# Performance work log

Hardware: AMD Instinct MI355X
Metric: run time of the kernel (lower is better)

## Reference

```python
import jax, jax.numpy as jnp
import numpy as np

BATCH = 64          # number of sequences
K = 4               # speculative tokens per sequence (uniform)
VOCAB = 128000


def setup_inputs() -> dict:
    key = jax.random.key(0)
    k1, k2 = jax.random.split(key)
    # total rows = BATCH * (K + 1): one bonus token per sequence
    logits = jax.random.normal(k1, (BATCH * (K + 1), VOCAB), dtype=jnp.float32)
    spec_token_ids = jax.random.randint(k2, (BATCH, K), 0, VOCAB, dtype=jnp.int32)
    return {"logits": logits, "spec_token_ids": spec_token_ids}


def reference(logits, spec_token_ids):
    """Greedy rejection sampling for speculative decoding.

    logits: [B*(K+1), V] -- target-model logits for K spec tokens + 1 bonus
    spec_token_ids: [B, K] int -- draft tokens
    Returns [B, K+1] int32 token ids, padded with -1 after the first rejection
    (equivalent to the ragged Python lists of the original, -1 = absent).
    """
    B, Kk = spec_token_ids.shape
    # [B, K+1] greedy tokens from the target model
    out_ids = jnp.argmax(logits, axis=-1).astype(jnp.int32).reshape(B, Kk + 1)
    # accept spec token i only if all tokens 0..i matched
    match = (spec_token_ids == out_ids[:, :Kk]).astype(jnp.int32)       # [B, K]
    accepted_prefix = jnp.cumprod(match, axis=1)                         # [B, K]
    # number of emitted tokens = accepted spec tokens + 1 (correction/bonus)
    num_emitted = accepted_prefix.sum(axis=1) + 1                        # [B]
    pos = jnp.arange(Kk + 1, dtype=jnp.int32)                            # [K+1]
    return jnp.where(pos[None, :] < num_emitted[:, None], out_ids, -1)
```

## Files before the change

### kernel.cpp

```cpp
#include <hip/hip_runtime.h>

#define BATCH 64
#define KSPEC 4
#define ROWS (BATCH * (KSPEC + 1))
#define VOCAB 128000
#define NVEC  (VOCAB / 4)
#define SEGS  8
#define SEGV  (NVEC / SEGS)

__device__ __forceinline__ unsigned long long make_key(float f, int idx) {
    unsigned int u = __float_as_uint(f);
    u ^= ((unsigned int)((int)u >> 31)) | 0x80000000u;
    return ((unsigned long long)u << 32) | (unsigned int)(~idx);
}

__device__ __forceinline__ unsigned long long umax64(unsigned long long a,
                                                     unsigned long long b) {
    return a > b ? a : b;
}

__global__ __launch_bounds__(256) void argmax_partial_kernel(
    const float* __restrict__ logits, unsigned long long* __restrict__ partials) {
    const int blk = blockIdx.x;
    const int row = blk >> 3;
    const int seg = blk & (SEGS - 1);
    const int tid = threadIdx.x;

    const float4* p = (const float4*)(logits + (long long)row * VOCAB) + seg * SEGV;
    const int base = seg * SEGV * 4;

    unsigned long long best = 0ull;
    for (int i = tid; i < SEGV; i += 256) {
        float4 v = p[i];
        int idx = base + i * 4;
        best = umax64(best, make_key(v.x, idx));
        best = umax64(best, make_key(v.y, idx + 1));
        best = umax64(best, make_key(v.z, idx + 2));
        best = umax64(best, make_key(v.w, idx + 3));
    }

    #pragma unroll
    for (int off = 32; off > 0; off >>= 1)
        best = umax64(best, __shfl_down(best, off, 64));

    __shared__ unsigned long long sk[4];
    const int wave = tid >> 6;
    const int lane = tid & 63;
    if (lane == 0) sk[wave] = best;
    __syncthreads();

    if (tid == 0) {
        best = umax64(umax64(sk[0], sk[1]), umax64(sk[2], sk[3]));
        partials[blk] = best;
    }
}

__global__ void finalize_kernel(const unsigned long long* __restrict__ partials,
                                const int* __restrict__ spec_ids,
                                int* __restrict__ out) {
    __shared__ int sidx[ROWS];
    const int t = threadIdx.x;

    if (t < ROWS) {
        unsigned long long best = partials[t * SEGS];
        #pragma unroll
        for (int j = 1; j < SEGS; j++)
            best = umax64(best, partials[t * SEGS + j]);
        sidx[t] = (int)(~(unsigned int)best);
    }
    __syncthreads();

    if (t < BATCH) {
        const int* ids = sidx + t * (KSPEC + 1);
        int num = 1;
        bool ok = true;
        #pragma unroll
        for (int i = 0; i < KSPEC; i++) {
            ok = ok && (spec_ids[t * KSPEC + i] == ids[i]);
            if (ok) num++;
        }
        #pragma unroll
        for (int i = 0; i <= KSPEC; i++)
            out[t * (KSPEC + 1) + i] = (i < num) ? ids[i] : -1;
    }
}

extern "C" void kernel_launch(void* const* d_in, const int* in_sizes, int n_in,
                              void* d_out, int out_size, void* d_ws, size_t ws_size,
                              hipStream_t stream) {
    const float* logits = (const float*)d_in[0];
    const int* spec_ids = (const int*)d_in[1];
    int* out            = (int*)d_out;
    unsigned long long* partials = (unsigned long long*)d_ws;

    argmax_partial_kernel<<<ROWS * SEGS, 256, 0, stream>>>(logits, partials);
    finalize_kernel<<<1, 384, 0, stream>>>(partials, spec_ids, out);
}
```

Before: 232.2 us.

## Compute argmax lazily per sequence, skipping rows after the first rejection

```diff
diff --git a/kernel.cpp b/kernel.cpp
--- a/kernel.cpp
+++ b/kernel.cpp
@@ -2,10 +2,11 @@
 
 #define BATCH 64
 #define KSPEC 4
-#define ROWS (BATCH * (KSPEC + 1))
+#define GROUP (KSPEC + 1)
+#define ROWS (BATCH * GROUP)
 #define VOCAB 128000
 #define NVEC  (VOCAB / 4)
-#define SEGS  8
+#define SEGS  16
 #define SEGV  (NVEC / SEGS)
 
 __device__ __forceinline__ unsigned long long make_key(float f, int idx) {
@@ -19,14 +20,15 @@
     return a > b ? a : b;
 }
 
-__global__ __launch_bounds__(256) void argmax_partial_kernel(
+__global__ __launch_bounds__(256) void argmax_first_rows_kernel(
     const float* __restrict__ logits, unsigned long long* __restrict__ partials) {
     const int blk = blockIdx.x;
-    const int row = blk >> 3;
+    const int b   = blk >> 4;
     const int seg = blk & (SEGS - 1);
     const int tid = threadIdx.x;
 
-    const float4* p = (const float4*)(logits + (long long)row * VOCAB) + seg * SEGV;
+    const long long row = (long long)b * GROUP;
+    const float4* p = (const float4*)(logits + row * VOCAB) + seg * SEGV;
     const int base = seg * SEGV * 4;
 
     unsigned long long best = 0ull;
@@ -45,8 +47,7 @@
 
     __shared__ unsigned long long sk[4];
     const int wave = tid >> 6;
-    const int lane = tid & 63;
-    if (lane == 0) sk[wave] = best;
+    if ((tid & 63) == 0) sk[wave] = best;
     __syncthreads();
 
     if (tid == 0) {
@@ -55,33 +56,60 @@
     }
 }
 
-__global__ void finalize_kernel(const unsigned long long* __restrict__ partials,
-                                const int* __restrict__ spec_ids,
-                                int* __restrict__ out) {
-    __shared__ int sidx[ROWS];
-    const int t = threadIdx.x;
+__global__ __launch_bounds__(1024) void finalize_kernel(
+    const float* __restrict__ logits,
+    const unsigned long long* __restrict__ partials,
+    const int* __restrict__ spec_ids,
+    int* __restrict__ out) {
+    const int b   = blockIdx.x;
+    const int tid = threadIdx.x;
 
-    if (t < ROWS) {
-        unsigned long long best = partials[t * SEGS];
+    __shared__ int ids[GROUP];
+    __shared__ int s_num;
+    __shared__ unsigned long long sk[16];
+
+    if (tid == 0) {
+        unsigned long long best = partials[b * SEGS];
         #pragma unroll
         for (int j = 1; j < SEGS; j++)
-            best = umax64(best, partials[t * SEGS + j]);
-        sidx[t] = (int)(~(unsigned int)best);
+            best = umax64(best, partials[b * SEGS + j]);
+        ids[0] = (int)(~(unsigned int)best);
+        s_num = 1;
     }
     __syncthreads();
 
-    if (t < BATCH) {
-        const int* ids = sidx + t * (KSPEC + 1);
-        int num = 1;
-        bool ok = true;
-        #pragma unroll
-        for (int i = 0; i < KSPEC; i++) {
-            ok = ok && (spec_ids[t * KSPEC + i] == ids[i]);
-            if (ok) num++;
+    bool ok = (spec_ids[b * KSPEC + 0] == ids[0]);
+    for (int i = 1; ok && i <= KSPEC; i++) {
+        const float4* p = (const float4*)(logits + ((long long)b * GROUP + i) * VOCAB);
+        unsigned long long best = 0ull;
+        for (int j = tid; j < NVEC; j += 1024) {
+            float4 v = p[j];
+            int idx = j * 4;
+            best = umax64(best, make_key(v.x, idx));
+            best = umax64(best, make_key(v.y, idx + 1));
+            best = umax64(best, make_key(v.z, idx + 2));
+            best = umax64(best, make_key(v.w, idx + 3));
         }
         #pragma unroll
-        for (int i = 0; i <= KSPEC; i++)
-            out[t * (KSPEC + 1) + i] = (i < num) ? ids[i] : -1;
+        for (int off = 32; off > 0; off >>= 1)
+            best = umax64(best, __shfl_down(best, off, 64));
+        if ((tid & 63) == 0) sk[tid >> 6] = best;
+        __syncthreads();
+        if (tid == 0) {
+            unsigned long long r = sk[0];
+            #pragma unroll
+            for (int w = 1; w < 16; w++) r = umax64(r, sk[w]);
+            ids[i] = (int)(~(unsigned int)r);
+            s_num = i + 1;
+        }
+        __syncthreads();
+        ok = (i < KSPEC) ? (spec_ids[b * KSPEC + i] == ids[i]) : false;
+        __syncthreads();
+    }
+
+    if (tid < GROUP) {
+        int num = s_num;
+        out[b * GROUP + tid] = (tid < num) ? ids[tid] : -1;
     }
 }
 
@@ -93,6 +121,6 @@
     int* out            = (int*)d_out;
     unsigned long long* partials = (unsigned long long*)d_ws;
 
-    argmax_partial_kernel<<<ROWS * SEGS, 256, 0, stream>>>(logits, partials);
-    finalize_kernel<<<1, 384, 0, stream>>>(partials, spec_ids, out);
+    argmax_first_rows_kernel<<<BATCH * SEGS, 256, 0, stream>>>(logits, partials);
+    finalize_kernel<<<BATCH, 1024, 0, stream>>>(logits, partials, spec_ids, out);
 }
```

Measured after the change: 198.3 us. -14.6%, faster.
